# Performance work log

Hardware: AMD Instinct MI355X
Metric: run time of the kernel (lower is better)

Reference implementation:

```python
import jax, jax.numpy as jnp
import numpy as np

B, N, C, H, NC = 8, 4096, 512, 256, 1000
GRID = 64  # N = GRID*GRID unique positions
LN_EPS = 1e-5


def setup_inputs() -> dict:
    key = jax.random.key(0)
    ks = jax.random.split(key, 10)
    # unique integer grid positions, same for every batch element (original order)
    i = jnp.arange(N)
    base = jnp.stack([i % GRID, i // GRID], axis=-1).astype(jnp.float32)  # [N,2]
    pos_org = jnp.broadcast_to(base, (B, N, 2))
    # per-batch random permutation -> shuffled positions (as the backbone would emit)
    perm = jax.vmap(lambda k: jax.random.permutation(k, N))(jax.random.split(ks[0], B))  # [B,N]
    pos_shuffled = jnp.take_along_axis(pos_org, perm[..., None], axis=1)
    s = 0.02
    return {
        "feat": jax.random.normal(ks[1], (B, N, C), jnp.float32),
        "prev_out": jax.random.normal(ks[2], (B, N, C), jnp.float32),
        "pos_org": pos_org,
        "pos_shuffled": pos_shuffled,
        "proj_W": jax.random.normal(ks[3], (C, C), jnp.float32) * s,
        "proj_b": jnp.zeros((C,), jnp.float32),
        "ln_g": jnp.ones((C,), jnp.float32),
        "ln_b": jnp.zeros((C,), jnp.float32),
        "W1": jax.random.normal(ks[4], (H, C), jnp.float32) * s,
        "b1": jnp.zeros((H,), jnp.float32),
        "W2": jax.random.normal(ks[5], (H, H), jnp.float32) * s,
        "b2": jnp.zeros((H,), jnp.float32),
        "W3": jax.random.normal(ks[6], (NC, H), jnp.float32) * s,
        "b3": jnp.zeros((NC,), jnp.float32),
    }


def _layernorm(x, g, b):
    x32 = x.astype(jnp.float32)
    mu = x32.mean(-1, keepdims=True)
    var = ((x32 - mu) ** 2).mean(-1, keepdims=True)
    return (x32 - mu) * jax.lax.rsqrt(var + LN_EPS) * g + b


def reference(feat, prev_out, pos_org, pos_shuffled, proj_W, proj_b,
              ln_g, ln_b, W1, b1, W2, b2, W3, b3):
    # find_pos_org_order: L1 cdist [B,N,N] + argmin over shuffled axis
    dists = jnp.abs(pos_org[:, :, None, :] - pos_shuffled[:, None, :, :]).sum(-1)
    pos_indices = jnp.argmin(dists, axis=2)  # [B,N]
    # batched gather: feat[b_, pos_indices]
    g = jnp.take_along_axis(feat, pos_indices[..., None], axis=1)  # [B,N,C]
    # fused proj -> layernorm (in fp32) -> cast back -> residual add
    proj = jnp.einsum('bnc,dc->bnd', g, proj_W) + proj_b
    out_feat = prev_out + _layernorm(proj, ln_g, ln_b).astype(feat.dtype)
    # mean-pool over tokens, 3-layer MLP head with relu on first two layers
    pooled = out_feat.mean(1)  # [B,C]
    h = jax.nn.relu(pooled @ W1.T + b1)
    h = jax.nn.relu(h @ W2.T + b2)
    return h @ W3.T + b3  # [B, num_classes]
```

## Files before the change

kernel.cpp:

```cpp
#include <hip/hip_runtime.h>
#include <stdint.h>

#define B_ 8
#define N_ 4096
#define C_ 512
#define H_ 256
#define NC_ 1000

typedef float v4f __attribute__((ext_vector_type(4)));
typedef short v8s __attribute__((ext_vector_type(8)));
typedef unsigned short ushort_t;

__device__ __forceinline__ uint32_t f2bf1(float f) {
    uint32_t u = __float_as_uint(f);
    return (u + 0x7FFFu + ((u >> 16) & 1u)) >> 16;
}
__device__ __forceinline__ uint32_t f2bf2(float lo, float hi) {
    return f2bf1(lo) | (f2bf1(hi) << 16);
}

__global__ void prep_kernel(const float* __restrict__ ps, const float* __restrict__ W,
                            int* __restrict__ inv, ushort_t* __restrict__ Wfrag) {
    int blk = blockIdx.x, t = threadIdx.x;
    if (blk < 128) {
        int gid = blk * 256 + t;
        float2 p = ((const float2*)ps)[gid];
        int key = (int)(p.x + 0.5f) + 64 * (int)(p.y + 0.5f);
        int b = gid >> 12;
        inv[(b << 12) + key] = gid & 4095;
    } else {
        int i = (blk - 128) * 256 + t;
        int d = i >> 6, kb = (i >> 2) & 15, q = i & 3;
        const float4* src = (const float4*)(W + d * C_ + kb * 32 + q * 8);
        float4 v0 = src[0], v1 = src[1];
        uint4 pk;
        pk.x = f2bf2(v0.x, v0.y); pk.y = f2bf2(v0.z, v0.w);
        pk.z = f2bf2(v1.x, v1.y); pk.w = f2bf2(v1.z, v1.w);
        ((uint4*)Wfrag)[((d >> 4) * 16 + kb) * 64 + q * 16 + (d & 15)] = pk;
    }
}

__global__ __launch_bounds__(512, 4)
void gemm_ln_pool(const float* __restrict__ feat, const float* __restrict__ prev,
                  const int* __restrict__ inv, const ushort_t* __restrict__ Wfrag,
                  const float* __restrict__ pb, const float* __restrict__ lg,
                  const float* __restrict__ lb, float* __restrict__ pooled) {
    __shared__ v8s Abuf[512];
    __shared__ float RowS[64], RowQ[64], ColS[512];

    const int t = threadIdx.x;
    const int b = blockIdx.x >> 6;
    const int row0 = (blockIdx.x & 63) << 6;
    const int wv = t >> 6, lane = t & 63, c = lane & 15, q = lane >> 4;

    if (t < 64) { RowS[t] = 0.f; RowQ[t] = 0.f; }

    const int arow = t >> 3;
    const int kcl = (t & 7) ^ (arow & 7);
    const int grow = inv[(b << 12) + row0 + arow];
    const float* asrc = feat + ((b * N_ + grow) * C_) + kcl * 8;

    const float* psrc = prev + ((b * N_ + row0) * C_) + t;
    float prevsum = 0.f;

    const ushort_t* fb[4];
#pragma unroll
    for (int nt = 0; nt < 4; nt++)
        fb[nt] = Wfrag + (wv * 4 + nt) * 8192 + lane * 8;

    v4f acc[4][4];
    const v4f vzero = {0.f, 0.f, 0.f, 0.f};
#pragma unroll
    for (int mt = 0; mt < 4; mt++)
#pragma unroll
        for (int nt = 0; nt < 4; nt++) acc[mt][nt] = vzero;

    for (int it = 0; it < 8; it++) {
        float4 f0 = ((const float4*)(asrc + it * 64))[0];
        float4 f1 = ((const float4*)(asrc + it * 64))[1];
#pragma unroll
        for (int rr = 0; rr < 8; rr++) prevsum += psrc[(it * 8 + rr) * C_];
        uint4 pk;
        pk.x = f2bf2(f0.x, f0.y); pk.y = f2bf2(f0.z, f0.w);
        pk.z = f2bf2(f1.x, f1.y); pk.w = f2bf2(f1.z, f1.w);
        ((uint4*)Abuf)[t] = pk;
        __syncthreads();

#pragma unroll
        for (int kk = 0; kk < 2; kk++) {
            const int kb = it * 2 + kk;
            v8s af[4], bf[4];
            const int ph = (kk * 4 + q) ^ (c & 7);
#pragma unroll
            for (int mt = 0; mt < 4; mt++) af[mt] = Abuf[mt * 128 + c * 8 + ph];
#pragma unroll
            for (int nt = 0; nt < 4; nt++)
                bf[nt] = *((const v8s*)(fb[nt] + kb * 512));
#pragma unroll
            for (int mt = 0; mt < 4; mt++)
#pragma unroll
                for (int nt = 0; nt < 4; nt++)
                    acc[mt][nt] = __builtin_amdgcn_mfma_f32_16x16x32_bf16(
                        af[mt], bf[nt], acc[mt][nt], 0, 0, 0);
        }
        __syncthreads();
    }

    float pb4[4], lg4[4], lb4[4];
#pragma unroll
    for (int nt = 0; nt < 4; nt++) {
        int n = wv * 64 + nt * 16 + c;
        pb4[nt] = pb[n]; lg4[nt] = lg[n]; lb4[nt] = lb[n];
    }
#pragma unroll
    for (int mt = 0; mt < 4; mt++) {
#pragma unroll
        for (int reg = 0; reg < 4; reg++) {
            float s1 = 0.f, s2 = 0.f;
#pragma unroll
            for (int nt = 0; nt < 4; nt++) {
                float v = acc[mt][nt][reg] + pb4[nt];
                acc[mt][nt][reg] = v;
                s1 += v; s2 += v * v;
            }
#pragma unroll
            for (int d = 1; d < 16; d <<= 1) {
                s1 += __shfl_xor(s1, d);
                s2 += __shfl_xor(s2, d);
            }
            if (c == 0) {
                int r = mt * 16 + q * 4 + reg;
                atomicAdd(&RowS[r], s1);
                atomicAdd(&RowQ[r], s2);
            }
        }
    }
    __syncthreads();
    if (t < 64) {
        float mu = RowS[t] * (1.f / C_);
        float var = RowQ[t] * (1.f / C_) - mu * mu;
        RowS[t] = mu;
        RowQ[t] = rsqrtf(var + 1e-5f);
    }
    __syncthreads();
    float col[4] = {0.f, 0.f, 0.f, 0.f};
#pragma unroll
    for (int mt = 0; mt < 4; mt++) {
#pragma unroll
        for (int reg = 0; reg < 4; reg++) {
            int r = mt * 16 + q * 4 + reg;
            float mu = RowS[r], rs = RowQ[r];
#pragma unroll
            for (int nt = 0; nt < 4; nt++)
                col[nt] += (acc[mt][nt][reg] - mu) * rs * lg4[nt] + lb4[nt];
        }
    }
#pragma unroll
    for (int nt = 0; nt < 4; nt++) {
        col[nt] += __shfl_xor(col[nt], 16);
        col[nt] += __shfl_xor(col[nt], 32);
    }
    if (lane < 16) {
#pragma unroll
        for (int nt = 0; nt < 4; nt++) ColS[wv * 64 + nt * 16 + c] = col[nt];
    }
    __syncthreads();
    atomicAdd(&pooled[b * C_ + t], ColS[t] + prevsum);
}

__global__ __launch_bounds__(256)
void head1(const float* __restrict__ pooled, const float* __restrict__ W1,
           const float* __restrict__ b1, float* __restrict__ h1) {
    const int t = threadIdx.x, wv = t >> 6, lane = t & 63;
    const int b = blockIdx.x >> 6;
    const int j = ((blockIdx.x & 63) << 2) + wv;
    const float4* wr = (const float4*)(W1 + j * C_);
    const float4* pr = (const float4*)(pooled + b * C_);
    float4 w0 = wr[lane], w1 = wr[lane + 64];
    float4 p0 = pr[lane], p1 = pr[lane + 64];
    float s = w0.x * p0.x + w0.y * p0.y + w0.z * p0.z + w0.w * p0.w
            + w1.x * p1.x + w1.y * p1.y + w1.z * p1.z + w1.w * p1.w;
#pragma unroll
    for (int d = 1; d < 64; d <<= 1) s += __shfl_xor(s, d);
    if (lane == 0) h1[b * H_ + j] = fmaxf(s * (1.f / 4096.f) + b1[j], 0.f);
}

__global__ __launch_bounds__(256)
void head2(const float* __restrict__ h1, const float* __restrict__ W2,
           const float* __restrict__ b2, float* __restrict__ h2) {
    const int t = threadIdx.x, wv = t >> 6, lane = t & 63;
    const int b = blockIdx.x >> 6;
    const int j = ((blockIdx.x & 63) << 2) + wv;
    float4 w0 = ((const float4*)(W2 + j * H_))[lane];
    float4 p0 = ((const float4*)(h1 + b * H_))[lane];
    float s = w0.x * p0.x + w0.y * p0.y + w0.z * p0.z + w0.w * p0.w;
#pragma unroll
    for (int d = 1; d < 64; d <<= 1) s += __shfl_xor(s, d);
    if (lane == 0) h2[b * H_ + j] = fmaxf(s + b2[j], 0.f);
}

__global__ __launch_bounds__(256)
void head3(const float* __restrict__ h2, const float* __restrict__ W3,
           const float* __restrict__ b3, float* __restrict__ out) {
    const int t = threadIdx.x, wv = t >> 6, lane = t & 63;
    const int b = blockIdx.x / 250;
    const int o = (blockIdx.x % 250) * 4 + wv;
    float4 w0 = ((const float4*)(W3 + o * H_))[lane];
    float4 p0 = ((const float4*)(h2 + b * H_))[lane];
    float s = w0.x * p0.x + w0.y * p0.y + w0.z * p0.z + w0.w * p0.w;
#pragma unroll
    for (int d = 1; d < 64; d <<= 1) s += __shfl_xor(s, d);
    if (lane == 0) out[b * NC_ + o] = s + b3[o];
}

extern "C" void kernel_launch(void* const* d_in, const int* in_sizes, int n_in,
                              void* d_out, int out_size, void* d_ws, size_t ws_size,
                              hipStream_t stream) {
    const float* feat  = (const float*)d_in[0];
    const float* prev  = (const float*)d_in[1];
    const float* ps    = (const float*)d_in[3];
    const float* projW = (const float*)d_in[4];
    const float* pb    = (const float*)d_in[5];
    const float* lg    = (const float*)d_in[6];
    const float* lb    = (const float*)d_in[7];
    const float* W1    = (const float*)d_in[8];
    const float* b1    = (const float*)d_in[9];
    const float* W2    = (const float*)d_in[10];
    const float* b2    = (const float*)d_in[11];
    const float* W3    = (const float*)d_in[12];
    const float* b3    = (const float*)d_in[13];
    float* out = (float*)d_out;

    char* ws = (char*)d_ws;
    ushort_t* Wfrag = (ushort_t*)ws;
    int* inv        = (int*)(ws + 524288);
    float* pooled   = (float*)(ws + 655360);
    float* h1       = (float*)(ws + 671744);
    float* h2       = (float*)(ws + 679936);

    hipMemsetAsync(pooled, 0, B_ * C_ * sizeof(float), stream);
    prep_kernel<<<256, 256, 0, stream>>>(ps, projW, inv, Wfrag);
    gemm_ln_pool<<<512, 512, 0, stream>>>(feat, prev, inv, Wfrag,
                                          pb, lg, lb, pooled);
    head1<<<512, 256, 0, stream>>>(pooled, W1, b1, h1);
    head2<<<512, 256, 0, stream>>>(h1, W2, b2, h2);
    head3<<<2000, 256, 0, stream>>>(h2, W3, b3, out);
}
```

Baseline: 241.7 us.

## Stage full A tile in LDS once, fuse head1/head2, fold memset into prep

The GEMM kernel now loads the whole gathered 64x512 bf16 A tile into a 64 KB LDS buffer up front and runs all 16 k-steps without per-iteration barriers. The prev_out row reads are interleaved into the k loop. The pooled-buffer memset is moved into prep_kernel, and head1/head2 are merged into one 8-block kernel that keeps intermediates in shared memory, cutting two launches. The larger LDS footprint lowers how many blocks fit per CU, which may reduce latency hiding for the global gather.

```diff
diff --git a/kernel.cpp b/kernel.cpp
--- a/kernel.cpp
+++ b/kernel.cpp
@@ -20,8 +20,14 @@
 }
 
 __global__ void prep_kernel(const float* __restrict__ ps, const float* __restrict__ W,
-                            int* __restrict__ inv, ushort_t* __restrict__ Wfrag) {
+                            int* __restrict__ inv, ushort_t* __restrict__ Wfrag,
+                            float* __restrict__ pooled) {
     int blk = blockIdx.x, t = threadIdx.x;
+    if (blk == 0) {
+        float4 z = {0.f, 0.f, 0.f, 0.f};
+#pragma unroll
+        for (int i = 0; i < 4; i++) ((float4*)pooled)[t * 4 + i] = z;
+    }
     if (blk < 128) {
         int gid = blk * 256 + t;
         float2 p = ((const float2*)ps)[gid];
@@ -45,7 +51,7 @@
                   const int* __restrict__ inv, const ushort_t* __restrict__ Wfrag,
                   const float* __restrict__ pb, const float* __restrict__ lg,
                   const float* __restrict__ lb, float* __restrict__ pooled) {
-    __shared__ v8s Abuf[512];
+    __shared__ v8s Abuf[4096];
     __shared__ float RowS[64], RowQ[64], ColS[512];
 
     const int t = threadIdx.x;
@@ -56,54 +62,54 @@
     if (t < 64) { RowS[t] = 0.f; RowQ[t] = 0.f; }
 
     const int arow = t >> 3;
-    const int kcl = (t & 7) ^ (arow & 7);
+    const int acol8 = t & 7;
     const int grow = inv[(b << 12) + row0 + arow];
-    const float* asrc = feat + ((b * N_ + grow) * C_) + kcl * 8;
-
-    const float* psrc = prev + ((b * N_ + row0) * C_) + t;
-    float prevsum = 0.f;
-
-    const ushort_t* fb[4];
-#pragma unroll
-    for (int nt = 0; nt < 4; nt++)
-        fb[nt] = Wfrag + (wv * 4 + nt) * 8192 + lane * 8;
-
-    v4f acc[4][4];
-    const v4f vzero = {0.f, 0.f, 0.f, 0.f};
-#pragma unroll
-    for (int mt = 0; mt < 4; mt++)
-#pragma unroll
-        for (int nt = 0; nt < 4; nt++) acc[mt][nt] = vzero;
-
-    for (int it = 0; it < 8; it++) {
-        float4 f0 = ((const float4*)(asrc + it * 64))[0];
-        float4 f1 = ((const float4*)(asrc + it * 64))[1];
-#pragma unroll
-        for (int rr = 0; rr < 8; rr++) prevsum += psrc[(it * 8 + rr) * C_];
+    const float* asrc = feat + ((size_t)(b * N_ + grow) * C_);
+#pragma unroll 4
+    for (int s = 0; s < 8; s++) {
+        const int chunk = s * 8 + acol8;
+        float4 f0 = ((const float4*)asrc)[chunk * 2];
+        float4 f1 = ((const float4*)asrc)[chunk * 2 + 1];
         uint4 pk;
         pk.x = f2bf2(f0.x, f0.y); pk.y = f2bf2(f0.z, f0.w);
         pk.z = f2bf2(f1.x, f1.y); pk.w = f2bf2(f1.z, f1.w);
-        ((uint4*)Abuf)[t] = pk;
-        __syncthreads();
-
-#pragma unroll
-        for (int kk = 0; kk < 2; kk++) {
-            const int kb = it * 2 + kk;
-            v8s af[4], bf[4];
-            const int ph = (kk * 4 + q) ^ (c & 7);
-#pragma unroll
-            for (int mt = 0; mt < 4; mt++) af[mt] = Abuf[mt * 128 + c * 8 + ph];
+        ((uint4*)Abuf)[arow * 64 + (chunk ^ (arow & 7))] = pk;
+    }
+
+    const ushort_t* fb[4];
+#pragma unroll
+    for (int nt = 0; nt < 4; nt++)
+        fb[nt] = Wfrag + (wv * 4 + nt) * 8192 + lane * 8;
+
+    const float* psrc = prev + ((b * N_ + row0) * C_) + t;
+    float prevsum = 0.f;
+
+    v4f acc[4][4];
+    const v4f vzero = {0.f, 0.f, 0.f, 0.f};
+#pragma unroll
+    for (int mt = 0; mt < 4; mt++)
+#pragma unroll
+        for (int nt = 0; nt < 4; nt++) acc[mt][nt] = vzero;
+
+    __syncthreads();
+
+#pragma unroll 2
+    for (int kb = 0; kb < 16; kb++) {
+        v8s af[4], bf[4];
+#pragma unroll
+        for (int nt = 0; nt < 4; nt++)
+            bf[nt] = *((const v8s*)(fb[nt] + kb * 512));
+#pragma unroll
+        for (int mt = 0; mt < 4; mt++)
+            af[mt] = Abuf[(mt * 16 + c) * 64 + ((kb * 4 + q) ^ (c & 7))];
+#pragma unroll
+        for (int rr = 0; rr < 4; rr++) prevsum += psrc[(kb * 4 + rr) * C_];
+#pragma unroll
+        for (int mt = 0; mt < 4; mt++)
 #pragma unroll
             for (int nt = 0; nt < 4; nt++)
-                bf[nt] = *((const v8s*)(fb[nt] + kb * 512));
-#pragma unroll
-            for (int mt = 0; mt < 4; mt++)
-#pragma unroll
-                for (int nt = 0; nt < 4; nt++)
-                    acc[mt][nt] = __builtin_amdgcn_mfma_f32_16x16x32_bf16(
-                        af[mt], bf[nt], acc[mt][nt], 0, 0, 0);
-        }
-        __syncthreads();
+                acc[mt][nt] = __builtin_amdgcn_mfma_f32_16x16x32_bf16(
+                    af[mt], bf[nt], acc[mt][nt], 0, 0, 0);
     }
 
     float pb4[4], lg4[4], lb4[4];
@@ -168,35 +174,42 @@
     atomicAdd(&pooled[b * C_ + t], ColS[t] + prevsum);
 }
 
-__global__ __launch_bounds__(256)
-void head1(const float* __restrict__ pooled, const float* __restrict__ W1,
-           const float* __restrict__ b1, float* __restrict__ h1) {
-    const int t = threadIdx.x, wv = t >> 6, lane = t & 63;
-    const int b = blockIdx.x >> 6;
-    const int j = ((blockIdx.x & 63) << 2) + wv;
-    const float4* wr = (const float4*)(W1 + j * C_);
-    const float4* pr = (const float4*)(pooled + b * C_);
-    float4 w0 = wr[lane], w1 = wr[lane + 64];
-    float4 p0 = pr[lane], p1 = pr[lane + 64];
-    float s = w0.x * p0.x + w0.y * p0.y + w0.z * p0.z + w0.w * p0.w
-            + w1.x * p1.x + w1.y * p1.y + w1.z * p1.z + w1.w * p1.w;
-#pragma unroll
-    for (int d = 1; d < 64; d <<= 1) s += __shfl_xor(s, d);
-    if (lane == 0) h1[b * H_ + j] = fmaxf(s * (1.f / 4096.f) + b1[j], 0.f);
-}
-
-__global__ __launch_bounds__(256)
-void head2(const float* __restrict__ h1, const float* __restrict__ W2,
-           const float* __restrict__ b2, float* __restrict__ h2) {
-    const int t = threadIdx.x, wv = t >> 6, lane = t & 63;
-    const int b = blockIdx.x >> 6;
-    const int j = ((blockIdx.x & 63) << 2) + wv;
-    float4 w0 = ((const float4*)(W2 + j * H_))[lane];
-    float4 p0 = ((const float4*)(h1 + b * H_))[lane];
-    float s = w0.x * p0.x + w0.y * p0.y + w0.z * p0.z + w0.w * p0.w;
-#pragma unroll
-    for (int d = 1; d < 64; d <<= 1) s += __shfl_xor(s, d);
-    if (lane == 0) h2[b * H_ + j] = fmaxf(s + b2[j], 0.f);
+__global__ __launch_bounds__(1024)
+void head12(const float* __restrict__ pooled,
+            const float* __restrict__ W1, const float* __restrict__ b1,
+            const float* __restrict__ W2, const float* __restrict__ b2,
+            float* __restrict__ h2out) {
+    __shared__ __align__(16) float P[512];
+    __shared__ __align__(16) float H1[256];
+    const int b = blockIdx.x, t = threadIdx.x, wv = t >> 6, lane = t & 63;
+
+    for (int i = t; i < 512; i += 1024) P[i] = pooled[b * 512 + i] * (1.f / 4096.f);
+    __syncthreads();
+
+#pragma unroll 2
+    for (int jj = 0; jj < 16; jj++) {
+        const int j = jj * 16 + wv;
+        const float4* wr = (const float4*)(W1 + j * C_);
+        float4 w0 = wr[lane], w1 = wr[lane + 64];
+        float4 p0 = ((const float4*)P)[lane], p1 = ((const float4*)P)[lane + 64];
+        float s = w0.x * p0.x + w0.y * p0.y + w0.z * p0.z + w0.w * p0.w
+                + w1.x * p1.x + w1.y * p1.y + w1.z * p1.z + w1.w * p1.w;
+#pragma unroll
+        for (int d = 1; d < 64; d <<= 1) s += __shfl_xor(s, d);
+        if (lane == 0) H1[j] = fmaxf(s + b1[j], 0.f);
+    }
+    __syncthreads();
+
+#pragma unroll 2
+    for (int jj = 0; jj < 16; jj++) {
+        const int j = jj * 16 + wv;
+        float4 w0 = ((const float4*)(W2 + j * H_))[lane];
+        float4 p0 = ((const float4*)H1)[lane];
+        float s = w0.x * p0.x + w0.y * p0.y + w0.z * p0.z + w0.w * p0.w;
+#pragma unroll
+        for (int d = 1; d < 64; d <<= 1) s += __shfl_xor(s, d);
+        if (lane == 0) h2out[b * H_ + j] = fmaxf(s + b2[j], 0.f);
+    }
 }
 
 __global__ __launch_bounds__(256)
@@ -235,14 +248,11 @@
     ushort_t* Wfrag = (ushort_t*)ws;
     int* inv        = (int*)(ws + 524288);
     float* pooled   = (float*)(ws + 655360);
-    float* h1       = (float*)(ws + 671744);
-    float* h2       = (float*)(ws + 679936);
-
-    hipMemsetAsync(pooled, 0, B_ * C_ * sizeof(float), stream);
-    prep_kernel<<<256, 256, 0, stream>>>(ps, projW, inv, Wfrag);
+    float* h2       = (float*)(ws + 671744);
+
+    prep_kernel<<<256, 256, 0, stream>>>(ps, projW, inv, Wfrag, pooled);
     gemm_ln_pool<<<512, 512, 0, stream>>>(feat, prev, inv, Wfrag,
                                           pb, lg, lb, pooled);
-    head1<<<512, 256, 0, stream>>>(pooled, W1, b1, h1);
-    head2<<<512, 256, 0, stream>>>(h1, W2, b2, h2);
+    head12<<<8, 1024, 0, stream>>>(pooled, W1, b1, W2, b2, h2);
     head3<<<2000, 256, 0, stream>>>(h2, W3, b3, out);
 }
```

After: 221.7 us. 8.3% less time.
